# Performance work log

Measured on AMD Instinct MI355X. Metric: run time of the kernel, lower is better.

## Reference

```python
import jax, jax.numpy as jnp
import numpy as np


def reference(x, edge_index, edge_attr, W, b):
    """PyG GCNConv: out = D^{-1/2} (A + I) D^{-1/2} X W + b.

    x: [N, Din] node features
    edge_index: [2, E] int (row=source, col=target)
    edge_attr: [E] edge weights
    W: [Din, Dout], b: [Dout]
    """
    N = x.shape[0]
    # add self-loops with weight 1 (PyG fill_value=1.0)
    loop = jnp.arange(N, dtype=edge_index.dtype)
    row = jnp.concatenate([edge_index[0], loop])
    col = jnp.concatenate([edge_index[1], loop])
    w = jnp.concatenate([edge_attr, jnp.ones((N,), dtype=edge_attr.dtype)])

    # symmetric normalization: norm_e = d[row]^-1/2 * w_e * d[col]^-1/2
    deg = jax.ops.segment_sum(w, col, num_segments=N)
    dis = jnp.where(deg > 0, jax.lax.rsqrt(jnp.where(deg > 0, deg, 1.0)), 0.0)
    norm = dis[row] * w * dis[col]

    # linear projection first (Din == Dout, cheaper either way), then
    # gather-scale-scatter aggregation at targets
    h = x @ W                                   # [N, Dout]
    msg = h[row] * norm[:, None]                # [E+N, Dout]
    out = jax.ops.segment_sum(msg, col, num_segments=N)  # [N, Dout]
    return out + b


def setup_inputs() -> dict:
    key = jax.random.key(0)
    k1, k2, k3, k4 = jax.random.split(key, 4)
    N, E, Din, Dout = 100000, 1600000, 128, 128
    x = jax.random.normal(k1, (N, Din), dtype=jnp.float32)
    edge_index = jax.random.randint(k2, (2, E), 0, N, dtype=jnp.int64)
    edge_attr = jax.random.uniform(k3, (E,), dtype=jnp.float32)
    # Glorot init like PyG Linear default
    W = jax.random.normal(k4, (Din, Dout), dtype=jnp.float32) * (1.0 / np.sqrt(Din))
    b = jnp.zeros((Dout,), dtype=jnp.float32)
    return {"x": x, "edge_index": edge_index, "edge_attr": edge_attr, "W": W, "b": b}
```

## Files before the change

### kernel.cpp

```cpp
#include <hip/hip_runtime.h>


#define ELEMS_PER_SCAN_BLOCK 4096
#define SCAN_SHIFT 12
#define CHUNK 2048
#define NCMAX 800

typedef __attribute__((ext_vector_type(8))) short short8;
typedef __attribute__((ext_vector_type(4))) float f32x4;

__device__ inline unsigned short f2bf(float f) {
    unsigned u = __float_as_uint(f);
    u += 0x7fffu + ((u >> 16) & 1u);
    return (unsigned short)(u >> 16);
}
__device__ inline float bf_lo(unsigned u) { return __uint_as_float(u << 16); }
__device__ inline float bf_hi(unsigned u) { return __uint_as_float(u & 0xffff0000u); }

__global__ void k_wprep(const float* __restrict__ W, unsigned short* __restrict__ Wtg) {
    int n = blockIdx.x;
    int k = threadIdx.x;
    Wtg[n * 128 + k] = f2bf(W[k * 128 + n]);
}

__device__ inline int wave_incl_scan(int x, int lane) {
    #pragma unroll
    for (int d = 1; d < 64; d <<= 1) {
        int y = __shfl_up(x, d, 64);
        if (lane >= d) x += y;
    }
    return x;
}

struct GSmem { short Xs[64][72]; short Ws[128][72]; };

__device__ __forceinline__ void gemm_body(GSmem& sm, const float* __restrict__ x,
                                          const unsigned short* __restrict__ Wtg,
                                          unsigned short* __restrict__ h,
                                          int row0, int N, int t) {
    int lane = t & 63, wid = t >> 6;
    int q = lane >> 4;
    int m = lane & 15;
    f32x4 acc[8];
    #pragma unroll
    for (int tde = 0; tde < 8; ++tde) acc[tde] = (f32x4){0.f, 0.f, 0.f, 0.f};

    #pragma unroll
    for (int kh = 0; kh < 2; ++kh) {
        {
            int r = t >> 2;
            int kf = (t & 3) * 16;
            int gr = row0 + r;
            const float4* src = (const float4*)(x + (size_t)gr * 128 + kh * 64 + kf);
            float4 a0 = make_float4(0.f, 0.f, 0.f, 0.f), a1 = a0, a2 = a0, a3 = a0;
            if (gr < N) { a0 = src[0]; a1 = src[1]; a2 = src[2]; a3 = src[3]; }
            short8 p0, p1;
            p0[0] = (short)f2bf(a0.x); p0[1] = (short)f2bf(a0.y);
            p0[2] = (short)f2bf(a0.z); p0[3] = (short)f2bf(a0.w);
            p0[4] = (short)f2bf(a1.x); p0[5] = (short)f2bf(a1.y);
            p0[6] = (short)f2bf(a1.z); p0[7] = (short)f2bf(a1.w);
            p1[0] = (short)f2bf(a2.x); p1[1] = (short)f2bf(a2.y);
            p1[2] = (short)f2bf(a2.z); p1[3] = (short)f2bf(a2.w);
            p1[4] = (short)f2bf(a3.x); p1[5] = (short)f2bf(a3.y);
            p1[6] = (short)f2bf(a3.z); p1[7] = (short)f2bf(a3.w);
            *(short8*)&sm.Xs[r][kf]     = p0;
            *(short8*)&sm.Xs[r][kf + 8] = p1;
        }
        {
            int n = t >> 1;
            int off = (t & 1) * 32;
            const short* wsrc = (const short*)Wtg + n * 128 + kh * 64 + off;
            #pragma unroll
            for (int i = 0; i < 4; ++i)
                *(short8*)&sm.Ws[n][off + 8 * i] = *(const short8*)(wsrc + 8 * i);
        }
        __syncthreads();
        #pragma unroll
        for (int kc = 0; kc < 64; kc += 32) {
            short8 af = *(const short8*)&sm.Xs[wid * 16 + m][kc + q * 8];
            #pragma unroll
            for (int tde = 0; tde < 8; ++tde) {
                short8 bf = *(const short8*)&sm.Ws[tde * 16 + m][kc + q * 8];
                acc[tde] = __builtin_amdgcn_mfma_f32_16x16x32_bf16(af, bf, acc[tde], 0, 0, 0);
            }
        }
        __syncthreads();
    }
    #pragma unroll
    for (int r = 0; r < 4; ++r) {
        int grow = row0 + wid * 16 + q * 4 + r;
        if (grow < N) {
            #pragma unroll
            for (int tde = 0; tde < 8; ++tde)
                h[(size_t)grow * 128 + tde * 16 + m] = f2bf(acc[tde][r]);
        }
    }
}

__global__ __launch_bounds__(256) void k_hist(const int* __restrict__ col,
                                              int* __restrict__ histg,
                                              const float* __restrict__ x,
                                              const unsigned short* __restrict__ Wtg,
                                              unsigned short* __restrict__ h,
                                              int E, int N, int NC, int NBLK, int gbase) {
    __shared__ union { int lh[1024]; GSmem g; } sm;
    int t = threadIdx.x;
    if ((int)blockIdx.x >= NBLK) {
        gemm_body(sm.g, x, Wtg, h, (gbase + (int)blockIdx.x - NBLK) * 64, N, t);
        return;
    }
    int blk = blockIdx.x;
    for (int i = t; i < 1024; i += 256) sm.lh[i] = 0;
    __syncthreads();
    int base = blk * CHUNK;
    #pragma unroll
    for (int i = 0; i < CHUNK / 256; ++i) {
        int e = base + i * 256 + t;
        if (e < E) atomicAdd(&sm.lh[col[e] >> 7], 1);
    }
    __syncthreads();
    for (int b = t; b < NC; b += 256) histg[b * NBLK + blk] = sm.lh[b];
}

__global__ void k_scan1(const int* __restrict__ in, int* __restrict__ out,
                        int* __restrict__ bsum, int M) {
    __shared__ int wsum[4];
    __shared__ int woff[4];
    int t = threadIdx.x, lane = t & 63, wid = t >> 6;
    int base = blockIdx.x * ELEMS_PER_SCAN_BLOCK + t * 16;
    int v[16];
    #pragma unroll
    for (int i = 0; i < 16; ++i) v[i] = (base + i < M) ? in[base + i] : 0;
    int run = 0;
    #pragma unroll
    for (int i = 0; i < 16; ++i) { int x = v[i]; v[i] = run; run += x; }
    int incl = wave_incl_scan(run, lane);
    int excl = incl - run;
    if (lane == 63) wsum[wid] = incl;
    __syncthreads();
    if (t == 0) {
        int r = 0;
        #pragma unroll
        for (int w = 0; w < 4; ++w) { int s = wsum[w]; woff[w] = r; r += s; }
        bsum[blockIdx.x] = r;
    }
    __syncthreads();
    int off = woff[wid] + excl;
    #pragma unroll
    for (int i = 0; i < 16; ++i)
        if (base + i < M) out[base + i] = v[i] + off;
}

__global__ void k_scan2(const int* __restrict__ bsum, int* __restrict__ boff, int NB) {
    __shared__ int wsum[4];
    __shared__ int woff[4];
    int t = threadIdx.x, lane = t & 63, wid = t >> 6;
    int x = (t < NB) ? bsum[t] : 0;
    int incl = wave_incl_scan(x, lane);
    int excl = incl - x;
    if (lane == 63) wsum[wid] = incl;
    __syncthreads();
    if (t == 0) {
        int r = 0;
        #pragma unroll
        for (int w = 0; w < 4; ++w) { int s = wsum[w]; woff[w] = r; r += s; }
    }
    __syncthreads();
    if (t < NB) boff[t] = woff[wid] + excl;
}

__global__ __launch_bounds__(256) void k_pg(const int* __restrict__ row,
                                            const int* __restrict__ col,
                                            const float* __restrict__ wgt,
                                            const int* __restrict__ histg,
                                            const int* __restrict__ boff,
                                            int2* __restrict__ srw,
                                            const float* __restrict__ x,
                                            const unsigned short* __restrict__ Wtg,
                                            unsigned short* __restrict__ h,
                                            int E, int N, int NC, int NBLK, int gbase) {
    __shared__ union {
        struct { int lcnt[NCMAX]; int gadj[NCMAX]; int2 stage[CHUNK]; int sdst[CHUNK];
                 int wsum[4]; int woff[4]; } p;
        GSmem g;
    } sm;
    int t = threadIdx.x;
    if ((int)blockIdx.x >= NBLK) {
        gemm_body(sm.g, x, Wtg, h, (gbase + (int)blockIdx.x - NBLK) * 64, N, t);
        return;
    }
    int blk = blockIdx.x;
    int lane = t & 63, wid = t >> 6;
    int base = blk * CHUNK;
    int nE = min(CHUNK, E - base);
    for (int b = t; b < NCMAX; b += 256) sm.p.lcnt[b] = 0;
    __syncthreads();
    #pragma unroll
    for (int i = 0; i < CHUNK / 256; ++i) {
        int e = base + i * 256 + t;
        if (e < E) atomicAdd(&sm.p.lcnt[col[e] >> 7], 1);
    }
    __syncthreads();
    int c4[4];
    int sum = 0;
    #pragma unroll
    for (int i = 0; i < 4; ++i) {
        int idx = t * 4 + i;
        int v = (idx < NCMAX) ? sm.p.lcnt[idx] : 0;
        c4[i] = sum; sum += v;
    }
    int incl = wave_incl_scan(sum, lane);
    int excl = incl - sum;
    if (lane == 63) sm.p.wsum[wid] = incl;
    __syncthreads();
    if (t == 0) {
        int r = 0;
        #pragma unroll
        for (int w = 0; w < 4; ++w) { int s = sm.p.wsum[w]; sm.p.woff[w] = r; r += s; }
    }
    __syncthreads();
    int tb = sm.p.woff[wid] + excl;
    __syncthreads();
    #pragma unroll
    for (int i = 0; i < 4; ++i) {
        int idx = t * 4 + i;
        if (idx < NCMAX) {
            int b0 = tb + c4[i];
            int gb = 0;
            if (idx < NC) {
                int g = idx * NBLK + blk;
                gb = histg[g] + boff[g >> SCAN_SHIFT];
            }
            sm.p.gadj[idx] = gb - b0;
            sm.p.lcnt[idx] = b0;
        }
    }
    __syncthreads();
    #pragma unroll
    for (int i = 0; i < CHUNK / 256; ++i) {
        int e = base + i * 256 + t;
        if (e < E) {
            int c = col[e];
            int slot = atomicAdd(&sm.p.lcnt[c >> 7], 1);
            sm.p.stage[slot] = make_int2(((c & 127) << 17) | row[e], __float_as_int(wgt[e]));
            sm.p.sdst[slot] = sm.p.gadj[c >> 7] + slot;
        }
    }
    __syncthreads();
    for (int s_ = t; s_ < nE; s_ += 256) {
        srw[sm.p.sdst[s_]] = sm.p.stage[s_];
    }
}

__global__ __launch_bounds__(256) void k_fine(const int* __restrict__ histg,
                                              const int* __restrict__ boff,
                                              const int2* __restrict__ srw,
                                              int* __restrict__ rowptr,
                                              float* __restrict__ dis,
                                              int2* __restrict__ spack,
                                              int E, int N, int NC, int NBLK) {
    __shared__ struct { int2 sbuf[3072]; int cnt128[128]; float degf[128];
                        int cur128[128]; int wtot[2]; } sf;
    int t = threadIdx.x, b = blockIdx.x;
    int nb = b << 7;
    int g0 = b * NBLK;
    int start = histg[g0] + boff[g0 >> SCAN_SHIFT];
    int end;
    if (b == NC - 1) end = E;
    else {
        int g1 = (b + 1) * NBLK;
        end = histg[g1] + boff[g1 >> SCAN_SHIFT];
    }
    int cnt = end - start;
    int NL = min(cnt, 3072);
    if (t < 128) { sf.cnt128[t] = 0; sf.degf[t] = 1.0f; }
    __syncthreads();
    for (int j = t; j < cnt; j += 256) {
        int2 s = srw[start + j];
        if (j < NL) sf.sbuf[j] = s;
        int c = s.x >> 17;
        atomicAdd(&sf.cnt128[c], 1);
        atomicAdd(&sf.degf[c], __int_as_float(s.y));
    }
    __syncthreads();
    int v = 0, incl = 0;
    if (t < 128) {
        v = sf.cnt128[t];
        incl = wave_incl_scan(v, t & 63);
        if ((t & 63) == 63) sf.wtot[t >> 6] = incl;
    }
    __syncthreads();
    if (t < 128) {
        int excl = incl - v + ((t >= 64) ? sf.wtot[0] : 0);
        int p = start + excl;
        sf.cur128[t] = p;
        int n = nb + t;
        if (n < N) {
            rowptr[n] = p;
            dis[n] = rsqrtf(sf.degf[t]);
        }
    }
    if (t == 0 && b == NC - 1) rowptr[N] = E;
    __syncthreads();
    for (int j = t; j < cnt; j += 256) {
        int2 s = (j < NL) ? sf.sbuf[j] : srw[start + j];
        int c = s.x >> 17;
        int pos = atomicAdd(&sf.cur128[c], 1);
        spack[pos] = make_int2(s.x & 0x1FFFF, s.y);
    }
}

__global__ __launch_bounds__(256) void k_gather(const unsigned int* __restrict__ hb,
                                                const float* __restrict__ dis,
                                                const int* __restrict__ rowptr,
                                                const long* __restrict__ spackl,
                                                const float* __restrict__ bias,
                                                float* __restrict__ out, int N) {
    int gid = blockIdx.x * blockDim.x + threadIdx.x;
    int node = gid >> 6;
    int lane = gid & 63;
    if (node >= N) return;
    node = __builtin_amdgcn_readfirstlane(node);

    float dn = dis[node];
    unsigned u = hb[(size_t)node * 64 + lane];
    float2 acc;
    acc.x = dn * bf_lo(u);
    acc.y = dn * bf_hi(u);

    int jb = rowptr[node], je = rowptr[node + 1];
    int j = jb;
    for (; j + 8 <= je; j += 8) {
        long q0 = __builtin_nontemporal_load(spackl + j);
        long q1 = __builtin_nontemporal_load(spackl + j + 1);
        long q2 = __builtin_nontemporal_load(spackl + j + 2);
        long q3 = __builtin_nontemporal_load(spackl + j + 3);
        long q4 = __builtin_nontemporal_load(spackl + j + 4);
        long q5 = __builtin_nontemporal_load(spackl + j + 5);
        long q6 = __builtin_nontemporal_load(spackl + j + 6);
        long q7 = __builtin_nontemporal_load(spackl + j + 7);
        int r0 = __builtin_amdgcn_readfirstlane((int)q0);
        int r1 = __builtin_amdgcn_readfirstlane((int)q1);
        int r2 = __builtin_amdgcn_readfirstlane((int)q2);
        int r3 = __builtin_amdgcn_readfirstlane((int)q3);
        int r4 = __builtin_amdgcn_readfirstlane((int)q4);
        int r5 = __builtin_amdgcn_readfirstlane((int)q5);
        int r6 = __builtin_amdgcn_readfirstlane((int)q6);
        int r7 = __builtin_amdgcn_readfirstlane((int)q7);
        unsigned u0 = hb[(size_t)r0 * 64 + lane];
        unsigned u1 = hb[(size_t)r1 * 64 + lane];
        unsigned u2 = hb[(size_t)r2 * 64 + lane];
        unsigned u3 = hb[(size_t)r3 * 64 + lane];
        unsigned u4 = hb[(size_t)r4 * 64 + lane];
        unsigned u5 = hb[(size_t)r5 * 64 + lane];
        unsigned u6 = hb[(size_t)r6 * 64 + lane];
        unsigned u7 = hb[(size_t)r7 * 64 + lane];
        float a0 = dis[r0] * __uint_as_float((unsigned)((unsigned long)q0 >> 32));
        float a1 = dis[r1] * __uint_as_float((unsigned)((unsigned long)q1 >> 32));
        float a2 = dis[r2] * __uint_as_float((unsigned)((unsigned long)q2 >> 32));
        float a3 = dis[r3] * __uint_as_float((unsigned)((unsigned long)q3 >> 32));
        float a4 = dis[r4] * __uint_as_float((unsigned)((unsigned long)q4 >> 32));
        float a5 = dis[r5] * __uint_as_float((unsigned)((unsigned long)q5 >> 32));
        float a6 = dis[r6] * __uint_as_float((unsigned)((unsigned long)q6 >> 32));
        float a7 = dis[r7] * __uint_as_float((unsigned)((unsigned long)q7 >> 32));
        acc.x = fmaf(a0, bf_lo(u0), acc.x); acc.y = fmaf(a0, bf_hi(u0), acc.y);
        acc.x = fmaf(a1, bf_lo(u1), acc.x); acc.y = fmaf(a1, bf_hi(u1), acc.y);
        acc.x = fmaf(a2, bf_lo(u2), acc.x); acc.y = fmaf(a2, bf_hi(u2), acc.y);
        acc.x = fmaf(a3, bf_lo(u3), acc.x); acc.y = fmaf(a3, bf_hi(u3), acc.y);
        acc.x = fmaf(a4, bf_lo(u4), acc.x); acc.y = fmaf(a4, bf_hi(u4), acc.y);
        acc.x = fmaf(a5, bf_lo(u5), acc.x); acc.y = fmaf(a5, bf_hi(u5), acc.y);
        acc.x = fmaf(a6, bf_lo(u6), acc.x); acc.y = fmaf(a6, bf_hi(u6), acc.y);
        acc.x = fmaf(a7, bf_lo(u7), acc.x); acc.y = fmaf(a7, bf_hi(u7), acc.y);
    }
    for (; j < je; ++j) {
        long q = __builtin_nontemporal_load(spackl + j);
        int r = __builtin_amdgcn_readfirstlane((int)q);
        unsigned uu = hb[(size_t)r * 64 + lane];
        float a = dis[r] * __uint_as_float((unsigned)((unsigned long)q >> 32));
        acc.x = fmaf(a, bf_lo(uu), acc.x);
        acc.y = fmaf(a, bf_hi(uu), acc.y);
    }

    int c0 = lane * 2;
    float2 bv = *(const float2*)(bias + c0);
    float2 o;
    o.x = bv.x + dn * acc.x;
    o.y = bv.y + dn * acc.y;
    union { float2 f; double d; } cvt;
    cvt.f = o;
    __builtin_nontemporal_store(cvt.d, (double*)(out + (size_t)node * 128 + c0));
}

extern "C" void kernel_launch(void* const* d_in, const int* in_sizes, int n_in,
                              void* d_out, int out_size, void* d_ws, size_t ws_size,
                              hipStream_t stream) {
    const float* x     = (const float*)d_in[0];
    const int*   eidx  = (const int*)d_in[1];
    const float* eattr = (const float*)d_in[2];
    const float* W     = (const float*)d_in[3];
    const float* bias  = (const float*)d_in[4];
    int N = in_sizes[0] / 128;
    int E = in_sizes[2];
    const int* row = eidx;
    const int* col = eidx + E;

    int NC = (N + 127) >> 7;
    int NBLK = (E + CHUNK - 1) / CHUNK;

    char* p = (char*)d_ws;
    auto carve = [&](size_t bytes) {
        char* q = p;
        p += (bytes + 255) & ~(size_t)255;
        return q;
    };
    unsigned short* h   = (unsigned short*)carve((size_t)N * 128 * sizeof(unsigned short));
    unsigned short* Wtg = (unsigned short*)carve(128 * 128 * sizeof(unsigned short));
    float* dis    = (float*)carve((size_t)N * sizeof(float));
    int*   rowptr = (int*)carve((size_t)(N + 1) * sizeof(int));
    int*   histg  = (int*)carve((size_t)NC * NBLK * sizeof(int));
    int2*  srw    = (int2*)carve((size_t)E * sizeof(int2));
    int2*  spack  = (int2*)carve((size_t)E * sizeof(int2));
    int*   bsum   = (int*)carve(256 * sizeof(int));
    int*   boff   = (int*)carve(256 * sizeof(int));

    int M = NC * NBLK;
    int NBs = (M + ELEMS_PER_SCAN_BLOCK - 1) / ELEMS_PER_SCAN_BLOCK;
    int GB  = (N + 63) / 64;
    int GB1 = GB / 2;
    int GB2 = GB - GB1;

    k_wprep<<<128, 128, 0, stream>>>(W, Wtg);
    k_hist<<<NBLK + GB1, 256, 0, stream>>>(col, histg, x, Wtg, h,
                                           E, N, NC, NBLK, 0);
    k_scan1<<<NBs, 256, 0, stream>>>(histg, histg, bsum, M);
    k_scan2<<<1, 256, 0, stream>>>(bsum, boff, NBs);
    k_pg<<<NBLK + GB2, 256, 0, stream>>>(row, col, eattr, histg, boff, srw,
                                         x, Wtg, h, E, N, NC, NBLK, GB1);
    k_fine<<<NC, 256, 0, stream>>>(histg, boff, srw, rowptr, dis, spack, E, N, NC, NBLK);
    {
        size_t threads = (size_t)N * 64;
        int blocks = (int)((threads + 255) / 256);
        k_gather<<<blocks, 256, 0, stream>>>((const unsigned int*)h, dis, rowptr,
                                             (const long*)spack, bias, (float*)d_out, N);
    }
}
```

Baseline: 255.2 us.

## Fold W prep into histogram and move GEMM halves into pg and fine kernels

```diff
diff --git a/kernel.cpp b/kernel.cpp
--- a/kernel.cpp
+++ b/kernel.cpp
@@ -17,10 +17,28 @@
 __device__ inline float bf_lo(unsigned u) { return __uint_as_float(u << 16); }
 __device__ inline float bf_hi(unsigned u) { return __uint_as_float(u & 0xffff0000u); }
 
-__global__ void k_wprep(const float* __restrict__ W, unsigned short* __restrict__ Wtg) {
-    int n = blockIdx.x;
-    int k = threadIdx.x;
-    Wtg[n * 128 + k] = f2bf(W[k * 128 + n]);
+__global__ __launch_bounds__(256) void k_hist(const int* __restrict__ col,
+                                              const float* __restrict__ W,
+                                              int* __restrict__ histg,
+                                              unsigned short* __restrict__ Wtg,
+                                              int E, int NC, int NBLK) {
+    __shared__ int lh[1024];
+    int t = threadIdx.x, blk = blockIdx.x;
+    if (blk < 64) {
+        int n = blk * 2 + (t >> 7);
+        int k = t & 127;
+        Wtg[n * 128 + k] = f2bf(W[k * 128 + n]);
+    }
+    for (int i = t; i < 1024; i += 256) lh[i] = 0;
+    __syncthreads();
+    int base = blk * CHUNK;
+    #pragma unroll
+    for (int i = 0; i < CHUNK / 256; ++i) {
+        int e = base + i * 256 + t;
+        if (e < E) atomicAdd(&lh[col[e] >> 7], 1);
+    }
+    __syncthreads();
+    for (int b = t; b < NC; b += 256) histg[b * NBLK + blk] = lh[b];
 }
 
 __device__ inline int wave_incl_scan(int x, int lane) {
@@ -30,6 +48,53 @@
         if (lane >= d) x += y;
     }
     return x;
+}
+
+__global__ void k_scan1(const int* __restrict__ in, int* __restrict__ out,
+                        int* __restrict__ bsum, int M) {
+    __shared__ int wsum[4];
+    __shared__ int woff[4];
+    int t = threadIdx.x, lane = t & 63, wid = t >> 6;
+    int base = blockIdx.x * ELEMS_PER_SCAN_BLOCK + t * 16;
+    int v[16];
+    #pragma unroll
+    for (int i = 0; i < 16; ++i) v[i] = (base + i < M) ? in[base + i] : 0;
+    int run = 0;
+    #pragma unroll
+    for (int i = 0; i < 16; ++i) { int x = v[i]; v[i] = run; run += x; }
+    int incl = wave_incl_scan(run, lane);
+    int excl = incl - run;
+    if (lane == 63) wsum[wid] = incl;
+    __syncthreads();
+    if (t == 0) {
+        int r = 0;
+        #pragma unroll
+        for (int w = 0; w < 4; ++w) { int s = wsum[w]; woff[w] = r; r += s; }
+        bsum[blockIdx.x] = r;
+    }
+    __syncthreads();
+    int off = woff[wid] + excl;
+    #pragma unroll
+    for (int i = 0; i < 16; ++i)
+        if (base + i < M) out[base + i] = v[i] + off;
+}
+
+__global__ void k_scan2(const int* __restrict__ bsum, int* __restrict__ boff, int NB) {
+    __shared__ int wsum[4];
+    __shared__ int woff[4];
+    int t = threadIdx.x, lane = t & 63, wid = t >> 6;
+    int x = (t < NB) ? bsum[t] : 0;
+    int incl = wave_incl_scan(x, lane);
+    int excl = incl - x;
+    if (lane == 63) wsum[wid] = incl;
+    __syncthreads();
+    if (t == 0) {
+        int r = 0;
+        #pragma unroll
+        for (int w = 0; w < 4; ++w) { int s = wsum[w]; woff[w] = r; r += s; }
+    }
+    __syncthreads();
+    if (t < NB) boff[t] = woff[wid] + excl;
 }
 
 struct GSmem { short Xs[64][72]; short Ws[128][72]; };
@@ -97,78 +162,6 @@
     }
 }
 
-__global__ __launch_bounds__(256) void k_hist(const int* __restrict__ col,
-                                              int* __restrict__ histg,
-                                              const float* __restrict__ x,
-                                              const unsigned short* __restrict__ Wtg,
-                                              unsigned short* __restrict__ h,
-                                              int E, int N, int NC, int NBLK, int gbase) {
-    __shared__ union { int lh[1024]; GSmem g; } sm;
-    int t = threadIdx.x;
-    if ((int)blockIdx.x >= NBLK) {
-        gemm_body(sm.g, x, Wtg, h, (gbase + (int)blockIdx.x - NBLK) * 64, N, t);
-        return;
-    }
-    int blk = blockIdx.x;
-    for (int i = t; i < 1024; i += 256) sm.lh[i] = 0;
-    __syncthreads();
-    int base = blk * CHUNK;
-    #pragma unroll
-    for (int i = 0; i < CHUNK / 256; ++i) {
-        int e = base + i * 256 + t;
-        if (e < E) atomicAdd(&sm.lh[col[e] >> 7], 1);
-    }
-    __syncthreads();
-    for (int b = t; b < NC; b += 256) histg[b * NBLK + blk] = sm.lh[b];
-}
-
-__global__ void k_scan1(const int* __restrict__ in, int* __restrict__ out,
-                        int* __restrict__ bsum, int M) {
-    __shared__ int wsum[4];
-    __shared__ int woff[4];
-    int t = threadIdx.x, lane = t & 63, wid = t >> 6;
-    int base = blockIdx.x * ELEMS_PER_SCAN_BLOCK + t * 16;
-    int v[16];
-    #pragma unroll
-    for (int i = 0; i < 16; ++i) v[i] = (base + i < M) ? in[base + i] : 0;
-    int run = 0;
-    #pragma unroll
-    for (int i = 0; i < 16; ++i) { int x = v[i]; v[i] = run; run += x; }
-    int incl = wave_incl_scan(run, lane);
-    int excl = incl - run;
-    if (lane == 63) wsum[wid] = incl;
-    __syncthreads();
-    if (t == 0) {
-        int r = 0;
-        #pragma unroll
-        for (int w = 0; w < 4; ++w) { int s = wsum[w]; woff[w] = r; r += s; }
-        bsum[blockIdx.x] = r;
-    }
-    __syncthreads();
-    int off = woff[wid] + excl;
-    #pragma unroll
-    for (int i = 0; i < 16; ++i)
-        if (base + i < M) out[base + i] = v[i] + off;
-}
-
-__global__ void k_scan2(const int* __restrict__ bsum, int* __restrict__ boff, int NB) {
-    __shared__ int wsum[4];
-    __shared__ int woff[4];
-    int t = threadIdx.x, lane = t & 63, wid = t >> 6;
-    int x = (t < NB) ? bsum[t] : 0;
-    int incl = wave_incl_scan(x, lane);
-    int excl = incl - x;
-    if (lane == 63) wsum[wid] = incl;
-    __syncthreads();
-    if (t == 0) {
-        int r = 0;
-        #pragma unroll
-        for (int w = 0; w < 4; ++w) { int s = wsum[w]; woff[w] = r; r += s; }
-    }
-    __syncthreads();
-    if (t < NB) boff[t] = woff[wid] + excl;
-}
-
 __global__ __launch_bounds__(256) void k_pg(const int* __restrict__ row,
                                             const int* __restrict__ col,
                                             const float* __restrict__ wgt,
@@ -258,10 +251,21 @@
                                               int* __restrict__ rowptr,
                                               float* __restrict__ dis,
                                               int2* __restrict__ spack,
-                                              int E, int N, int NC, int NBLK) {
-    __shared__ struct { int2 sbuf[3072]; int cnt128[128]; float degf[128];
-                        int cur128[128]; int wtot[2]; } sf;
-    int t = threadIdx.x, b = blockIdx.x;
+                                              const float* __restrict__ x,
+                                              const unsigned short* __restrict__ Wtg,
+                                              unsigned short* __restrict__ h,
+                                              int E, int N, int NC, int NBLK, int gbase) {
+    __shared__ union {
+        struct { int2 sbuf[3072]; int cnt128[128]; float degf[128];
+                 int cur128[128]; int wtot[2]; } f;
+        GSmem g;
+    } sm;
+    int t = threadIdx.x;
+    if ((int)blockIdx.x >= NC) {
+        gemm_body(sm.g, x, Wtg, h, (gbase + (int)blockIdx.x - NC) * 64, N, t);
+        return;
+    }
+    int b = blockIdx.x;
     int nb = b << 7;
     int g0 = b * NBLK;
     int start = histg[g0] + boff[g0 >> SCAN_SHIFT];
@@ -273,39 +277,39 @@
     }
     int cnt = end - start;
     int NL = min(cnt, 3072);
-    if (t < 128) { sf.cnt128[t] = 0; sf.degf[t] = 1.0f; }
+    if (t < 128) { sm.f.cnt128[t] = 0; sm.f.degf[t] = 1.0f; }
     __syncthreads();
     for (int j = t; j < cnt; j += 256) {
         int2 s = srw[start + j];
-        if (j < NL) sf.sbuf[j] = s;
+        if (j < NL) sm.f.sbuf[j] = s;
         int c = s.x >> 17;
-        atomicAdd(&sf.cnt128[c], 1);
-        atomicAdd(&sf.degf[c], __int_as_float(s.y));
+        atomicAdd(&sm.f.cnt128[c], 1);
+        atomicAdd(&sm.f.degf[c], __int_as_float(s.y));
     }
     __syncthreads();
     int v = 0, incl = 0;
     if (t < 128) {
-        v = sf.cnt128[t];
+        v = sm.f.cnt128[t];
         incl = wave_incl_scan(v, t & 63);
-        if ((t & 63) == 63) sf.wtot[t >> 6] = incl;
+        if ((t & 63) == 63) sm.f.wtot[t >> 6] = incl;
     }
     __syncthreads();
     if (t < 128) {
-        int excl = incl - v + ((t >= 64) ? sf.wtot[0] : 0);
+        int excl = incl - v + ((t >= 64) ? sm.f.wtot[0] : 0);
         int p = start + excl;
-        sf.cur128[t] = p;
+        sm.f.cur128[t] = p;
         int n = nb + t;
         if (n < N) {
             rowptr[n] = p;
-            dis[n] = rsqrtf(sf.degf[t]);
+            dis[n] = rsqrtf(sm.f.degf[t]);
         }
     }
     if (t == 0 && b == NC - 1) rowptr[N] = E;
     __syncthreads();
     for (int j = t; j < cnt; j += 256) {
-        int2 s = (j < NL) ? sf.sbuf[j] : srw[start + j];
+        int2 s = (j < NL) ? sm.f.sbuf[j] : srw[start + j];
         int c = s.x >> 17;
-        int pos = atomicAdd(&sf.cur128[c], 1);
+        int pos = atomicAdd(&sm.f.cur128[c], 1);
         spack[pos] = make_int2(s.x & 0x1FFFF, s.y);
     }
 }
@@ -429,14 +433,13 @@
     int GB1 = GB / 2;
     int GB2 = GB - GB1;
 
-    k_wprep<<<128, 128, 0, stream>>>(W, Wtg);
-    k_hist<<<NBLK + GB1, 256, 0, stream>>>(col, histg, x, Wtg, h,
-                                           E, N, NC, NBLK, 0);
+    k_hist<<<NBLK, 256, 0, stream>>>(col, W, histg, Wtg, E, NC, NBLK);
     k_scan1<<<NBs, 256, 0, stream>>>(histg, histg, bsum, M);
     k_scan2<<<1, 256, 0, stream>>>(bsum, boff, NBs);
-    k_pg<<<NBLK + GB2, 256, 0, stream>>>(row, col, eattr, histg, boff, srw,
+    k_pg<<<NBLK + GB1, 256, 0, stream>>>(row, col, eattr, histg, boff, srw,
+                                         x, Wtg, h, E, N, NC, NBLK, 0);
+    k_fine<<<NC + GB2, 256, 0, stream>>>(histg, boff, srw, rowptr, dis, spack,
                                          x, Wtg, h, E, N, NC, NBLK, GB1);
-    k_fine<<<NC, 256, 0, stream>>>(histg, boff, srw, rowptr, dis, spack, E, N, NC, NBLK);
     {
         size_t threads = (size_t)N * 64;
         int blocks = (int)((threads + 255) / 256);
```

Measured after the change: 251.7 us. About the same (-1.4%).
